# Kernel optimization log

Hardware: AMD Instinct MI355X
Metric: run time of the kernel (lower is better)

## Reference

```python
import jax, jax.numpy as jnp
import numpy as np

B, S, D, E, TOP_K = 4, 4096, 2048, 64, 2


def setup_inputs() -> dict:
    key = jax.random.key(0)
    kx, kw, kb = jax.random.split(key, 3)
    x = jax.random.normal(kx, (B, S, D), dtype=jnp.float32)
    # nn.Linear(d_model, n_expert): weight (E, D), bias (E,)
    bound = 1.0 / np.sqrt(D)
    W = jax.random.uniform(kw, (E, D), dtype=jnp.float32, minval=-bound, maxval=bound)
    b = jax.random.uniform(kb, (E,), dtype=jnp.float32, minval=-bound, maxval=bound)
    return {"x": x, "W": W, "b": b}


def reference(x, W, b):
    # logits: (B, S, E)
    logits = jnp.einsum("bsd,ed->bse", x, W) + b
    top_k_logits, ids = jax.lax.top_k(logits, TOP_K)  # (B,S,K) each
    # scatter top-k logits into a -inf filled tensor along the expert dim
    n = B * S
    flat = jnp.full((n, E), -jnp.inf, dtype=logits.dtype)
    rows = jnp.arange(n)[:, None]  # (n,1)
    flat = flat.at[rows, ids.reshape(n, TOP_K)].set(top_k_logits.reshape(n, TOP_K))
    sparse_logits = flat.reshape(B, S, E)
    router_output = jax.nn.softmax(sparse_logits, axis=-1)  # zeros outside top-k
    return router_output, ids
```

## Files before the change

### kernel.cpp

```cpp
#include <hip/hip_runtime.h>
#include <math.h>

#define NTOK 16384
#define D_   2048
#define E_   64
#define TPB  64
#define NKC  (D_/32)

typedef _Float16 f16x8 __attribute__((ext_vector_type(8)));
typedef float    f32x4 __attribute__((ext_vector_type(4)));

#define LSCALE      256.0f
#define LSCALE2_INV (1.0f/65536.0f)

#define BUF_BYTES   16384
#define LOG_STRIDE  65
#define RES_OFF_F   (TPB*LOG_STRIDE)
#define SMEM_FLOATS 16384

__global__ __launch_bounds__(256)
void prep_w(const float* __restrict__ W,
            _Float16* __restrict__ wh, _Float16* __restrict__ wl)
{
    const int idx = blockIdx.x * 256 + threadIdx.x;
    const int l  = idx & 63;
    const int kc = (idx >> 6) & 63;
    const int nt = idx >> 12;
    const int e  = nt * 16 + (l & 15);
    const int g  = l >> 4;
    const float* src = W + (size_t)e * D_ + kc * 32 + g * 4;
    const float4 f0 = *reinterpret_cast<const float4*>(src);
    const float4 f1 = *reinterpret_cast<const float4*>(src + 16);
    const float v[8] = {f0.x, f0.y, f0.z, f0.w, f1.x, f1.y, f1.z, f1.w};
    f16x8 h, lo;
#pragma unroll
    for (int j = 0; j < 8; ++j) {
        const float vs = v[j] * LSCALE;
        const _Float16 hj = (_Float16)vs;
        h[j]  = hj;
        lo[j] = (_Float16)(vs - (float)hj);
    }
    *reinterpret_cast<f16x8*>(wh + (size_t)idx * 8) = h;
    *reinterpret_cast<f16x8*>(wl + (size_t)idx * 8) = lo;
}

__device__ __forceinline__ void stage16(const void* g, void* l) {
    __builtin_amdgcn_global_load_lds(
        (const __attribute__((address_space(1))) void*)g,
        (__attribute__((address_space(3))) void*)l, 16, 0, 0);
}

__global__ __launch_bounds__(512, 4)
void router_mfma(const float* __restrict__ x,
                 const _Float16* __restrict__ wh,
                 const _Float16* __restrict__ wl,
                 const float* __restrict__ bias,
                 float* __restrict__ out)
{
    __shared__ float smem[SMEM_FLOATS];
    char* sb = (char*)smem;

    const int tid = threadIdx.x;
    const int l   = tid & 63;
    const int w   = __builtin_amdgcn_readfirstlane(tid >> 6);
    const int mt  = w >> 1;
    const int nt0 = (w & 1) * 2;
    const int nt1 = nt0 + 1;
    const int T0  = blockIdx.x * TPB;
    const int g   = l >> 4;

    f32x4 acc0 = {0.f, 0.f, 0.f, 0.f};
    f32x4 acc1 = {0.f, 0.f, 0.f, 0.f};

    const int srow  = (w << 3) + (l >> 3);
    const int sslot = (l & 7) ^ (srow & 7);
    const float* xsrc0 = x + (size_t)(T0 + srow) * D_ + sslot * 4;
    const int bnt = w & 3;
    const _Float16* bsrc0 =
        (w < 4 ? wh : wl) + ((size_t)bnt * NKC * 64 + l) * 8;
    const int xdst_off = (w << 10);
    const int bdst_off = (w < 4 ? 8192 : 12288) + (bnt << 10);

    auto STAGE = [&](int kc) {
        char* bb = sb + (kc & 3) * BUF_BYTES;
        stage16(xsrc0 + kc * 32,          bb + xdst_off);
        stage16(bsrc0 + (size_t)kc * 512, bb + bdst_off);
    };

    const int arow = mt * 16 + (l & 15);
    const int r7   = arow & 7;
    const int xa_off = arow * 128 + ((g       ^ r7) << 4);
    const int xb_off = arow * 128 + (((4 + g) ^ r7) << 4);

    auto COMPUTE = [&](int kc) {
        const char* bb = sb + (kc & 3) * BUF_BYTES;
        const float4 xa = *reinterpret_cast<const float4*>(bb + xa_off);
        const float4 xb = *reinterpret_cast<const float4*>(bb + xb_off);
        const f16x8 bh0 = *reinterpret_cast<const f16x8*>(bb + 8192  + nt0 * 1024 + (l << 4));
        const f16x8 bl0 = *reinterpret_cast<const f16x8*>(bb + 12288 + nt0 * 1024 + (l << 4));
        const f16x8 bh1 = *reinterpret_cast<const f16x8*>(bb + 8192  + nt1 * 1024 + (l << 4));
        const f16x8 bl1 = *reinterpret_cast<const f16x8*>(bb + 12288 + nt1 * 1024 + (l << 4));
        const float av[8] = {xa.x, xa.y, xa.z, xa.w, xb.x, xb.y, xb.z, xb.w};
        f16x8 ah, al_;
#pragma unroll
        for (int j = 0; j < 8; ++j) {
            const float vs = av[j] * LSCALE;
            const _Float16 hj = (_Float16)vs;
            ah[j]  = hj;
            al_[j] = (_Float16)(vs - (float)hj);
        }
        acc0 = __builtin_amdgcn_mfma_f32_16x16x32_f16(ah,  bh0, acc0, 0, 0, 0);
        acc0 = __builtin_amdgcn_mfma_f32_16x16x32_f16(al_, bh0, acc0, 0, 0, 0);
        acc0 = __builtin_amdgcn_mfma_f32_16x16x32_f16(ah,  bl0, acc0, 0, 0, 0);
        acc1 = __builtin_amdgcn_mfma_f32_16x16x32_f16(ah,  bh1, acc1, 0, 0, 0);
        acc1 = __builtin_amdgcn_mfma_f32_16x16x32_f16(al_, bh1, acc1, 0, 0, 0);
        acc1 = __builtin_amdgcn_mfma_f32_16x16x32_f16(ah,  bl1, acc1, 0, 0, 0);
    };

    STAGE(0); STAGE(1); STAGE(2);
    for (int kc = 0; kc < NKC - 3; ++kc) {
        asm volatile("s_waitcnt vmcnt(4)" ::: "memory");
        __builtin_amdgcn_s_barrier();
        STAGE(kc + 3);
        COMPUTE(kc);
    }
    asm volatile("s_waitcnt vmcnt(4)" ::: "memory");
    __builtin_amdgcn_s_barrier();
    COMPUTE(NKC - 3);
    asm volatile("s_waitcnt vmcnt(2)" ::: "memory");
    __builtin_amdgcn_s_barrier();
    COMPUTE(NKC - 2);
    asm volatile("s_waitcnt vmcnt(0)" ::: "memory");
    __builtin_amdgcn_s_barrier();
    COMPUTE(NKC - 1);

    {
        float* logits = smem;
        const int row0 = mt * 16 + g * 4;
        const int c0   = nt0 * 16 + (l & 15);
        const int c1   = nt1 * 16 + (l & 15);
#pragma unroll
        for (int r = 0; r < 4; ++r) {
            logits[(row0 + r) * LOG_STRIDE + c0] = acc0[r] * LSCALE2_INV;
            logits[(row0 + r) * LOG_STRIDE + c1] = acc1[r] * LSCALE2_INV;
        }
    }
    __syncthreads();

    float* res = smem + RES_OFF_F;
    if (tid < TPB) {
        const float* lg = smem + tid * LOG_STRIDE;
        float m1 = -INFINITY, m2 = -INFINITY;
        int i1 = 0, i2 = 0;
        for (int e = 0; e < E_; ++e) {
            const float v = lg[e] + bias[e];
            if (v > m1)      { m2 = m1; i2 = i1; m1 = v; i1 = e; }
            else if (v > m2) { m2 = v;  i2 = e; }
        }
        const float ex  = expf(m2 - m1);
        const float den = 1.f + ex;
        res[tid*4+0] = 1.f / den;
        res[tid*4+1] = ex / den;
        res[tid*4+2] = (float)i1;
        res[tid*4+3] = (float)i2;
    }
    __syncthreads();

    const size_t obase = (size_t)T0 * E_;
#pragma unroll
    for (int i = 0; i < (TPB * E_) / 512; ++i) {
        const int f = i * 512 + tid;
        const int t = f >> 6;
        const int e = f & 63;
        const float p1 = res[t*4+0];
        const float p2 = res[t*4+1];
        const int   i1 = (int)res[t*4+2];
        const int   i2 = (int)res[t*4+3];
        float v = 0.f;
        if (e == i1)      v = p1;
        else if (e == i2) v = p2;
        out[obase + f] = v;
    }
    if (tid < TPB * 2) {
        out[(size_t)NTOK * E_ + (size_t)T0 * 2 + tid] =
            res[(tid >> 1) * 4 + 2 + (tid & 1)];
    }
}

extern "C" void kernel_launch(void* const* d_in, const int* in_sizes, int n_in,
                              void* d_out, int out_size, void* d_ws, size_t ws_size,
                              hipStream_t stream) {
    const float* x = (const float*)d_in[0];
    const float* W = (const float*)d_in[1];
    const float* b = (const float*)d_in[2];
    float* out     = (float*)d_out;
    _Float16* wh   = (_Float16*)d_ws;
    _Float16* wl   = wh + (size_t)4 * NKC * 64 * 8;

    hipLaunchKernelGGL(prep_w, dim3(64), dim3(256), 0, stream, W, wh, wl);
    hipLaunchKernelGGL(router_mfma, dim3(NTOK / TPB), dim3(512), 0, stream,
                       x, wh, wl, b, out);
}
```

Measured before the change: 59.96 us.

## Halve tokens per block, register-prefetch W fragments, stage x in 4-chunk supersteps

Tokens per block drop from 64 to 32, which doubles the grid, and each wave now owns a single 16x16 output tile. The W hi/lo fragments are no longer staged through LDS. They are loaded from global straight into registers with one superstep of double-buffered prefetch. x is staged into LDS four k-chunks at a time, so there is one barrier per superstep instead of one per chunk. The aim is to cut barrier and LDS traffic and raise occupancy and parallelism, at the cost of more register pressure and repeated global or L2 reads of W across more blocks.

```diff
diff --git a/kernel.cpp b/kernel.cpp
--- a/kernel.cpp
+++ b/kernel.cpp
@@ -4,8 +4,9 @@
 #define NTOK 16384
 #define D_   2048
 #define E_   64
-#define TPB  64
+#define TPB  32
 #define NKC  (D_/32)
+#define NS   16
 
 typedef _Float16 f16x8 __attribute__((ext_vector_type(8)));
 typedef float    f32x4 __attribute__((ext_vector_type(4)));
@@ -13,7 +14,6 @@
 #define LSCALE      256.0f
 #define LSCALE2_INV (1.0f/65536.0f)
 
-#define BUF_BYTES   16384
 #define LOG_STRIDE  65
 #define RES_OFF_F   (TPB*LOG_STRIDE)
 #define SMEM_FLOATS 16384
@@ -63,87 +63,89 @@
     const int tid = threadIdx.x;
     const int l   = tid & 63;
     const int w   = __builtin_amdgcn_readfirstlane(tid >> 6);
-    const int mt  = w >> 1;
-    const int nt0 = (w & 1) * 2;
-    const int nt1 = nt0 + 1;
+    const int mt  = w >> 2;
+    const int nt  = w & 3;
     const int T0  = blockIdx.x * TPB;
     const int g   = l >> 4;
 
-    f32x4 acc0 = {0.f, 0.f, 0.f, 0.f};
-    f32x4 acc1 = {0.f, 0.f, 0.f, 0.f};
-
-    const int srow  = (w << 3) + (l >> 3);
-    const int sslot = (l & 7) ^ (srow & 7);
-    const float* xsrc0 = x + (size_t)(T0 + srow) * D_ + sslot * 4;
-    const int bnt = w & 3;
-    const _Float16* bsrc0 =
-        (w < 4 ? wh : wl) + ((size_t)bnt * NKC * 64 + l) * 8;
-    const int xdst_off = (w << 10);
-    const int bdst_off = (w < 4 ? 8192 : 12288) + (bnt << 10);
-
-    auto STAGE = [&](int kc) {
-        char* bb = sb + (kc & 3) * BUF_BYTES;
-        stage16(xsrc0 + kc * 32,          bb + xdst_off);
-        stage16(bsrc0 + (size_t)kc * 512, bb + bdst_off);
+    f32x4 acc = {0.f, 0.f, 0.f, 0.f};
+
+    const int c1   = 512 + tid;
+    const int row0 = (tid >> 3) & 31, slot0 = (tid & 7) ^ (row0 & 7);
+    const int row1 = (c1  >> 3) & 31, slot1 = (c1  & 7) ^ (row1 & 7);
+    const float* xs0 = x + (size_t)(T0 + row0) * D_ + (tid >> 8) * 32 + slot0 * 4;
+    const float* xs1 = x + (size_t)(T0 + row1) * D_ + (c1  >> 8) * 32 + slot1 * 4;
+
+    auto STAGE_X = [&](int sup) {
+        const int bo = (sup & 3) << 14;
+        stage16(xs0 + (size_t)sup * 128, sb + bo + (w << 10));
+        stage16(xs1 + (size_t)sup * 128, sb + bo + 8192 + (w << 10));
     };
 
-    const int arow = mt * 16 + (l & 15);
-    const int r7   = arow & 7;
-    const int xa_off = arow * 128 + ((g       ^ r7) << 4);
-    const int xb_off = arow * 128 + (((4 + g) ^ r7) << 4);
-
-    auto COMPUTE = [&](int kc) {
-        const char* bb = sb + (kc & 3) * BUF_BYTES;
-        const float4 xa = *reinterpret_cast<const float4*>(bb + xa_off);
-        const float4 xb = *reinterpret_cast<const float4*>(bb + xb_off);
-        const f16x8 bh0 = *reinterpret_cast<const f16x8*>(bb + 8192  + nt0 * 1024 + (l << 4));
-        const f16x8 bl0 = *reinterpret_cast<const f16x8*>(bb + 12288 + nt0 * 1024 + (l << 4));
-        const f16x8 bh1 = *reinterpret_cast<const f16x8*>(bb + 8192  + nt1 * 1024 + (l << 4));
-        const f16x8 bl1 = *reinterpret_cast<const f16x8*>(bb + 12288 + nt1 * 1024 + (l << 4));
-        const float av[8] = {xa.x, xa.y, xa.z, xa.w, xb.x, xb.y, xb.z, xb.w};
+    const _Float16* bh_base = wh + ((size_t)nt * NKC * 64 + l) * 8;
+    const _Float16* bl_base = wl + ((size_t)nt * NKC * 64 + l) * 8;
+    auto LDB_H = [&](int kc) { return *reinterpret_cast<const f16x8*>(bh_base + (size_t)kc * 512); };
+    auto LDB_L = [&](int kc) { return *reinterpret_cast<const f16x8*>(bl_base + (size_t)kc * 512); };
+
+    const int arow   = mt * 16 + (l & 15);
+    const int r7_    = arow & 7;
+    const int xa_off = arow * 128 + ((g       ^ r7_) << 4);
+    const int xb_off = arow * 128 + (((4 + g) ^ r7_) << 4);
+
+    auto COMPUTE = [&](int pb, f16x8 bh, f16x8 bl) {
+        const float4 xa = *reinterpret_cast<const float4*>(sb + pb + xa_off);
+        const float4 xb = *reinterpret_cast<const float4*>(sb + pb + xb_off);
         f16x8 ah, al_;
-#pragma unroll
-        for (int j = 0; j < 8; ++j) {
-            const float vs = av[j] * LSCALE;
-            const _Float16 hj = (_Float16)vs;
-            ah[j]  = hj;
-            al_[j] = (_Float16)(vs - (float)hj);
-        }
-        acc0 = __builtin_amdgcn_mfma_f32_16x16x32_f16(ah,  bh0, acc0, 0, 0, 0);
-        acc0 = __builtin_amdgcn_mfma_f32_16x16x32_f16(al_, bh0, acc0, 0, 0, 0);
-        acc0 = __builtin_amdgcn_mfma_f32_16x16x32_f16(ah,  bl0, acc0, 0, 0, 0);
-        acc1 = __builtin_amdgcn_mfma_f32_16x16x32_f16(ah,  bh1, acc1, 0, 0, 0);
-        acc1 = __builtin_amdgcn_mfma_f32_16x16x32_f16(al_, bh1, acc1, 0, 0, 0);
-        acc1 = __builtin_amdgcn_mfma_f32_16x16x32_f16(ah,  bl1, acc1, 0, 0, 0);
+        {
+            float vs;
+            vs = xa.x * LSCALE; ah[0] = (_Float16)vs; al_[0] = (_Float16)(vs - (float)ah[0]);
+            vs = xa.y * LSCALE; ah[1] = (_Float16)vs; al_[1] = (_Float16)(vs - (float)ah[1]);
+            vs = xa.z * LSCALE; ah[2] = (_Float16)vs; al_[2] = (_Float16)(vs - (float)ah[2]);
+            vs = xa.w * LSCALE; ah[3] = (_Float16)vs; al_[3] = (_Float16)(vs - (float)ah[3]);
+            vs = xb.x * LSCALE; ah[4] = (_Float16)vs; al_[4] = (_Float16)(vs - (float)ah[4]);
+            vs = xb.y * LSCALE; ah[5] = (_Float16)vs; al_[5] = (_Float16)(vs - (float)ah[5]);
+            vs = xb.z * LSCALE; ah[6] = (_Float16)vs; al_[6] = (_Float16)(vs - (float)ah[6]);
+            vs = xb.w * LSCALE; ah[7] = (_Float16)vs; al_[7] = (_Float16)(vs - (float)ah[7]);
+        }
+        acc = __builtin_amdgcn_mfma_f32_16x16x32_f16(ah,  bh, acc, 0, 0, 0);
+        acc = __builtin_amdgcn_mfma_f32_16x16x32_f16(al_, bh, acc, 0, 0, 0);
+        acc = __builtin_amdgcn_mfma_f32_16x16x32_f16(ah,  bl, acc, 0, 0, 0);
     };
 
-    STAGE(0); STAGE(1); STAGE(2);
-    for (int kc = 0; kc < NKC - 3; ++kc) {
-        asm volatile("s_waitcnt vmcnt(4)" ::: "memory");
-        __builtin_amdgcn_s_barrier();
-        STAGE(kc + 3);
-        COMPUTE(kc);
-    }
+    f16x8 bhc[4], blc[4], bhn[4], bln[4];
+#pragma unroll
+    for (int j = 0; j < 4; ++j) { bhc[j] = LDB_H(j); blc[j] = LDB_L(j); }
+    STAGE_X(0); STAGE_X(1); STAGE_X(2);
     asm volatile("s_waitcnt vmcnt(4)" ::: "memory");
     __builtin_amdgcn_s_barrier();
-    COMPUTE(NKC - 3);
-    asm volatile("s_waitcnt vmcnt(2)" ::: "memory");
-    __builtin_amdgcn_s_barrier();
-    COMPUTE(NKC - 2);
-    asm volatile("s_waitcnt vmcnt(0)" ::: "memory");
-    __builtin_amdgcn_s_barrier();
-    COMPUTE(NKC - 1);
+
+    for (int s = 0; s < NS; ++s) {
+        const int K  = s << 2;
+        const int bo = (s & 3) << 14;
+        if (s < NS - 1) {
+#pragma unroll
+            for (int j = 0; j < 4; ++j) { bhn[j] = LDB_H(K + 4 + j); bln[j] = LDB_L(K + 4 + j); }
+        }
+        COMPUTE(bo,         bhc[0], blc[0]);
+        COMPUTE(bo | 4096,  bhc[1], blc[1]);
+        COMPUTE(bo | 8192,  bhc[2], blc[2]);
+        COMPUTE(bo | 12288, bhc[3], blc[3]);
+        if (s + 3 < NS) STAGE_X(s + 3);
+        if (s < NS - 1) {
+#pragma unroll
+            for (int j = 0; j < 4; ++j) { bhc[j] = bhn[j]; blc[j] = bln[j]; }
+            asm volatile("s_waitcnt vmcnt(10)" ::: "memory");
+            __builtin_amdgcn_s_barrier();
+        }
+    }
 
     {
         float* logits = smem;
-        const int row0 = mt * 16 + g * 4;
-        const int c0   = nt0 * 16 + (l & 15);
-        const int c1   = nt1 * 16 + (l & 15);
-#pragma unroll
-        for (int r = 0; r < 4; ++r) {
-            logits[(row0 + r) * LOG_STRIDE + c0] = acc0[r] * LSCALE2_INV;
-            logits[(row0 + r) * LOG_STRIDE + c1] = acc1[r] * LSCALE2_INV;
-        }
+        const int rr0 = mt * 16 + g * 4;
+        const int cc  = nt * 16 + (l & 15);
+#pragma unroll
+        for (int r = 0; r < 4; ++r)
+            logits[(rr0 + r) * LOG_STRIDE + cc] = acc[r] * LSCALE2_INV;
     }
     __syncthreads();
 
```

New measurement: 59.74 us. Within noise of the previous version (-0.4%).
